# Optimization experiments

Measured on AMD Instinct MI355X. Metric: run time of the kernel, lower is better.

Reference implementation:

```python
import jax, jax.numpy as jnp
import numpy as np

B, T = 32, 4096
ATTN_DIM, ENC_DIM, DEC_DIM = 128, 512, 1024


def setup_inputs() -> dict:
    key = jax.random.key(0)
    k1, k2, k3, k4, k5, k6 = jax.random.split(key, 6)
    return {
        "query": jax.random.normal(k1, (B, DEC_DIM), dtype=jnp.float32),
        "memory": jax.random.normal(k2, (B, T, ENC_DIM), dtype=jnp.float32),
        "attention_weights_cum": jax.random.uniform(k3, (B, T), dtype=jnp.float32),
        "Wq": jax.random.normal(k4, (DEC_DIM, ATTN_DIM), dtype=jnp.float32) * (1.0 / np.sqrt(DEC_DIM)),
        "Wm": jax.random.normal(k5, (ENC_DIM, ATTN_DIM), dtype=jnp.float32) * (1.0 / np.sqrt(ENC_DIM)),
        "v": jax.random.normal(k6, (ATTN_DIM,), dtype=jnp.float32),
    }


def reference(query, memory, attention_weights_cum, Wq, Wm, v):
    # processed_query: [B, 1, A]; processed_memory: [B, T, A]
    pq = jnp.einsum('bd,da->ba', query, Wq)[:, None, :]
    pm = jnp.einsum('bte,ea->bta', memory, Wm)
    # scores: [B, T] = sum_a tanh(pq + pm) * v
    scores = jnp.einsum('bta,a->bt', jnp.tanh(pq + pm), v)
    alignments = jax.nn.softmax(scores, axis=-1)  # [B, T]
    context = jnp.einsum('bt,bte->be', alignments, memory)  # [B, E]
    return context, alignments
```

## Files before the change

### kernel.cpp

```cpp
#include <hip/hip_runtime.h>
#include <hip/hip_bf16.h>
#include <math.h>

#define B_SZ 32
#define T_SZ 4096
#define A_SZ 128
#define E_SZ 512
#define D_SZ 1024

typedef __attribute__((ext_vector_type(8))) short short8;
typedef __attribute__((ext_vector_type(4))) float f32x4;

static __device__ __forceinline__ unsigned short f32_to_bf16_rne(float x) {
    unsigned int u = __float_as_uint(x);
    unsigned int r = (u + 0x7fffu + ((u >> 16) & 1u)) >> 16;
    return (unsigned short)r;
}
static __device__ __forceinline__ float bf16_to_f32(unsigned short h) {
    return __uint_as_float(((unsigned int)h) << 16);
}

__global__ __launch_bounds__(256) void k_prep(const float* __restrict__ q,
                                              const float* __restrict__ Wq,
                                              const float* __restrict__ Wm,
                                              float* __restrict__ pq,
                                              unsigned short* __restrict__ WmTh,
                                              unsigned short* __restrict__ WmTl,
                                              float* __restrict__ ctx_out) {
    const int tid = threadIdx.x;
    if (blockIdx.x < 32) {
        const int b = blockIdx.x;
        __shared__ float ql[D_SZ];
        #pragma unroll
        for (int s = 0; s < D_SZ / 256; ++s)
            ql[s * 256 + tid] = q[b * D_SZ + s * 256 + tid];
        __syncthreads();
        if (tid < A_SZ) {
            const int a = tid;
            float acc = 0.f;
            #pragma unroll 8
            for (int d = 0; d < D_SZ; ++d)
                acc = fmaf(ql[d], Wq[d * A_SZ + a], acc);
            pq[b * A_SZ + a] = acc;
            *(float4*)(ctx_out + (size_t)b * E_SZ + tid * 4) =
                make_float4(0.f, 0.f, 0.f, 0.f);
        }
    } else {
        const int a = blockIdx.x - 32;
        for (int e = tid; e < E_SZ; e += 256) {
            float x = Wm[(size_t)e * A_SZ + a];
            unsigned short h = f32_to_bf16_rne(x);
            float r = x - bf16_to_f32(h);
            unsigned short l = f32_to_bf16_rne(r);
            WmTh[(size_t)a * E_SZ + e] = h;
            WmTl[(size_t)a * E_SZ + e] = l;
        }
    }
}

#define LDST 72

__global__ __launch_bounds__(256, 2) void k_scores_mfma(
    const float* __restrict__ mem,
    const unsigned short* __restrict__ WmTh,
    const unsigned short* __restrict__ WmTl,
    const float* __restrict__ pq,
    const float* __restrict__ v,
    float* __restrict__ scores) {
    __shared__ unsigned short Ah[128 * LDST];
    __shared__ unsigned short Al[128 * LDST];

    const int b = blockIdx.y;
    const int t0 = blockIdx.x * 128;
    const int tid = threadIdx.x;
    const int w = tid >> 6;
    const int lane = tid & 63;
    const int l16 = lane & 15;
    const int lk = lane >> 4;

    const float* memB = mem + ((size_t)b * T_SZ + t0) * E_SZ;

    float pqr[8], vr[8];
    #pragma unroll
    for (int n = 0; n < 8; ++n) {
        pqr[n] = pq[b * A_SZ + n * 16 + l16];
        vr[n]  = v[n * 16 + l16];
    }

    f32x4 acc[2][8];
    #pragma unroll
    for (int m = 0; m < 2; ++m)
        #pragma unroll
        for (int n = 0; n < 8; ++n)
            acc[m][n] = (f32x4){0.f, 0.f, 0.f, 0.f};

    for (int c = 0; c < 8; ++c) {
        const int e0 = c * 64;
        __syncthreads();
        #pragma unroll
        for (int s = 0; s < 8; ++s) {
            int idx = s * 256 + tid;
            int row = idx >> 4;
            int e4  = (idx & 15) << 2;
            float4 val = *(const float4*)(memB + (size_t)row * E_SZ + e0 + e4);
            float xs[4] = {val.x, val.y, val.z, val.w};
            unsigned int hp[2], lp[2];
            unsigned short h0 = f32_to_bf16_rne(xs[0]);
            unsigned short h1 = f32_to_bf16_rne(xs[1]);
            unsigned short h2 = f32_to_bf16_rne(xs[2]);
            unsigned short h3 = f32_to_bf16_rne(xs[3]);
            hp[0] = (unsigned int)h0 | ((unsigned int)h1 << 16);
            hp[1] = (unsigned int)h2 | ((unsigned int)h3 << 16);
            unsigned short l0 = f32_to_bf16_rne(xs[0] - bf16_to_f32(h0));
            unsigned short l1 = f32_to_bf16_rne(xs[1] - bf16_to_f32(h1));
            unsigned short l2 = f32_to_bf16_rne(xs[2] - bf16_to_f32(h2));
            unsigned short l3 = f32_to_bf16_rne(xs[3] - bf16_to_f32(h3));
            lp[0] = (unsigned int)l0 | ((unsigned int)l1 << 16);
            lp[1] = (unsigned int)l2 | ((unsigned int)l3 << 16);
            *(uint2*)&Ah[row * LDST + e4] = make_uint2(hp[0], hp[1]);
            *(uint2*)&Al[row * LDST + e4] = make_uint2(lp[0], lp[1]);
        }
        __syncthreads();

        #pragma unroll
        for (int kk = 0; kk < 2; ++kk) {
            short8 ah[2], al[2];
            #pragma unroll
            for (int m = 0; m < 2; ++m) {
                int row = w * 32 + m * 16 + l16;
                int off = row * LDST + kk * 32 + lk * 8;
                ah[m] = *(const short8*)&Ah[off];
                al[m] = *(const short8*)&Al[off];
            }
            const int eb = e0 + kk * 32 + lk * 8;
            #pragma unroll
            for (int n = 0; n < 8; ++n) {
                const int a = n * 16 + l16;
                short8 bh = *(const short8*)&WmTh[(size_t)a * E_SZ + eb];
                short8 bl = *(const short8*)&WmTl[(size_t)a * E_SZ + eb];
                acc[0][n] = __builtin_amdgcn_mfma_f32_16x16x32_bf16(ah[0], bh, acc[0][n], 0, 0, 0);
                acc[1][n] = __builtin_amdgcn_mfma_f32_16x16x32_bf16(ah[1], bh, acc[1][n], 0, 0, 0);
                acc[0][n] = __builtin_amdgcn_mfma_f32_16x16x32_bf16(al[0], bh, acc[0][n], 0, 0, 0);
                acc[1][n] = __builtin_amdgcn_mfma_f32_16x16x32_bf16(al[1], bh, acc[1][n], 0, 0, 0);
                acc[0][n] = __builtin_amdgcn_mfma_f32_16x16x32_bf16(ah[0], bl, acc[0][n], 0, 0, 0);
                acc[1][n] = __builtin_amdgcn_mfma_f32_16x16x32_bf16(ah[1], bl, acc[1][n], 0, 0, 0);
            }
        }
    }

    #pragma unroll
    for (int m = 0; m < 2; ++m) {
        float part[4] = {0.f, 0.f, 0.f, 0.f};
        #pragma unroll
        for (int n = 0; n < 8; ++n)
            #pragma unroll
            for (int r = 0; r < 4; ++r)
                part[r] += tanhf(pqr[n] + acc[m][n][r]) * vr[n];
        #pragma unroll
        for (int r = 0; r < 4; ++r) {
            #pragma unroll
            for (int off = 1; off < 16; off <<= 1)
                part[r] += __shfl_xor(part[r], off);
        }
        if (l16 == 0) {
            const int t = t0 + w * 32 + m * 16 + lk * 4;
            #pragma unroll
            for (int r = 0; r < 4; ++r)
                scores[(size_t)b * T_SZ + t + r] = part[r];
        }
    }
}

__global__ __launch_bounds__(256) void k_softmax(float* __restrict__ sc) {
    const int b = blockIdx.x;
    const int tid = threadIdx.x;
    float* row = sc + (size_t)b * T_SZ;

    float4 v4[4];
    float mx = -1e30f;
    #pragma unroll
    for (int s = 0; s < 4; ++s) {
        v4[s] = *(float4*)&row[(s * 256 + tid) * 4];
        mx = fmaxf(mx, fmaxf(fmaxf(v4[s].x, v4[s].y), fmaxf(v4[s].z, v4[s].w)));
    }
    #pragma unroll
    for (int off = 1; off < 64; off <<= 1)
        mx = fmaxf(mx, __shfl_xor(mx, off));
    __shared__ float redm[4], reds[4];
    const int wid = tid >> 6, lane = tid & 63;
    if (lane == 0) redm[wid] = mx;
    __syncthreads();
    mx = fmaxf(fmaxf(redm[0], redm[1]), fmaxf(redm[2], redm[3]));

    float sum = 0.f;
    #pragma unroll
    for (int s = 0; s < 4; ++s) {
        v4[s].x = __expf(v4[s].x - mx);
        v4[s].y = __expf(v4[s].y - mx);
        v4[s].z = __expf(v4[s].z - mx);
        v4[s].w = __expf(v4[s].w - mx);
        sum += v4[s].x + v4[s].y + v4[s].z + v4[s].w;
    }
    #pragma unroll
    for (int off = 1; off < 64; off <<= 1)
        sum += __shfl_xor(sum, off);
    if (lane == 0) reds[wid] = sum;
    __syncthreads();
    const float inv = 1.f / (reds[0] + reds[1] + reds[2] + reds[3]);
    #pragma unroll
    for (int s = 0; s < 4; ++s) {
        v4[s].x *= inv; v4[s].y *= inv; v4[s].z *= inv; v4[s].w *= inv;
        *(float4*)&row[(s * 256 + tid) * 4] = v4[s];
    }
}

__global__ __launch_bounds__(256) void k_ctx(const float* __restrict__ mem,
                                             const float* __restrict__ align,
                                             float* __restrict__ ctx) {
    const int b  = blockIdx.y;
    const int t0 = blockIdx.x * 128;
    const int tid = threadIdx.x;
    __shared__ float al[128];
    if (tid < 128) al[tid] = align[(size_t)b * T_SZ + t0 + tid];
    __syncthreads();

    const float* memB = mem + ((size_t)b * T_SZ + t0) * E_SZ;
    const int e4 = (tid & 127) * 4;
    const int th = tid >> 7;
    float4 acc = make_float4(0.f, 0.f, 0.f, 0.f);
    #pragma unroll 4
    for (int t = th; t < 128; t += 2) {
        float4 m = *(const float4*)(memB + (size_t)t * E_SZ + e4);
        const float wgt = al[t];
        acc.x = fmaf(wgt, m.x, acc.x);
        acc.y = fmaf(wgt, m.y, acc.y);
        acc.z = fmaf(wgt, m.z, acc.z);
        acc.w = fmaf(wgt, m.w, acc.w);
    }
    float* c = ctx + (size_t)b * E_SZ + e4;
    atomicAdd(c + 0, acc.x);
    atomicAdd(c + 1, acc.y);
    atomicAdd(c + 2, acc.z);
    atomicAdd(c + 3, acc.w);
}

extern "C" void kernel_launch(void* const* d_in, const int* in_sizes, int n_in,
                              void* d_out, int out_size, void* d_ws, size_t ws_size,
                              hipStream_t stream) {
    const float* query  = (const float*)d_in[0];
    const float* memory = (const float*)d_in[1];
    const float* Wq     = (const float*)d_in[3];
    const float* Wm     = (const float*)d_in[4];
    const float* v      = (const float*)d_in[5];

    float* ctx_out   = (float*)d_out;
    float* align_out = (float*)d_out + B_SZ * E_SZ;

    char* ws = (char*)d_ws;
    float* pq            = (float*)ws;
    unsigned short* WmTh = (unsigned short*)(ws + 16 * 1024);
    unsigned short* WmTl = (unsigned short*)(ws + 160 * 1024);

    k_prep<<<160, 256, 0, stream>>>(query, Wq, Wm, pq, WmTh, WmTl, ctx_out);
    k_scores_mfma<<<dim3(T_SZ / 128, B_SZ), 256, 0, stream>>>(memory, WmTh, WmTl, pq, v, align_out);
    k_softmax<<<B_SZ, 256, 0, stream>>>(align_out);
    k_ctx<<<dim3(T_SZ / 128, B_SZ), 256, 0, stream>>>(memory, align_out, ctx_out);
}
```

Baseline: 555.1 us.

## Fuse scores, chunk softmax and context into one pass with split-softmax combine

Merges the score GEMM, a per-chunk online softmax and the context accumulation into one kernel, so each 128-row memory tile is read while still hot in cache instead of being streamed again by a separate context kernel. A small combine kernel rescales the per-chunk partial contexts and normalizes the alignments, which replaces the atomics and the standalone softmax. It also stages the Wm hi/lo operands in LDS with a smaller K chunk and a higher occupancy target, and swaps tanhf for an exp-based tanh. The cost is extra workspace traffic for the partial contexts and a slightly less accurate tanh.

Result: faster. 501.8 us (-9.6%).

```diff
diff --git a/kernel.cpp b/kernel.cpp
--- a/kernel.cpp
+++ b/kernel.cpp
@@ -7,6 +7,7 @@
 #define A_SZ 128
 #define E_SZ 512
 #define D_SZ 1024
+#define NCH  32
 
 typedef __attribute__((ext_vector_type(8))) short short8;
 typedef __attribute__((ext_vector_type(4))) float f32x4;
@@ -18,6 +19,12 @@
 }
 static __device__ __forceinline__ float bf16_to_f32(unsigned short h) {
     return __uint_as_float(((unsigned int)h) << 16);
+}
+static __device__ __forceinline__ float tanh_fast(float x) {
+    float ax = fabsf(x);
+    float e  = __expf(2.f * ax);
+    float r  = 1.f - 2.f / (e + 1.f);
+    return __builtin_copysignf(r, x);
 }
 
 __global__ __launch_bounds__(256) void k_prep(const float* __restrict__ q,
@@ -25,8 +32,7 @@
                                               const float* __restrict__ Wm,
                                               float* __restrict__ pq,
                                               unsigned short* __restrict__ WmTh,
-                                              unsigned short* __restrict__ WmTl,
-                                              float* __restrict__ ctx_out) {
+                                              unsigned short* __restrict__ WmTl) {
     const int tid = threadIdx.x;
     if (blockIdx.x < 32) {
         const int b = blockIdx.x;
@@ -42,8 +48,6 @@
             for (int d = 0; d < D_SZ; ++d)
                 acc = fmaf(ql[d], Wq[d * A_SZ + a], acc);
             pq[b * A_SZ + a] = acc;
-            *(float4*)(ctx_out + (size_t)b * E_SZ + tid * 4) =
-                make_float4(0.f, 0.f, 0.f, 0.f);
         }
     } else {
         const int a = blockIdx.x - 32;
@@ -58,20 +62,30 @@
     }
 }
 
-#define LDST 72
-
-__global__ __launch_bounds__(256, 2) void k_scores_mfma(
+#define AST 36
+#define BST 40
+
+__global__ __launch_bounds__(256, 4) void k_fused(
     const float* __restrict__ mem,
     const unsigned short* __restrict__ WmTh,
     const unsigned short* __restrict__ WmTl,
     const float* __restrict__ pq,
     const float* __restrict__ v,
-    float* __restrict__ scores) {
-    __shared__ unsigned short Ah[128 * LDST];
-    __shared__ unsigned short Al[128 * LDST];
-
-    const int b = blockIdx.y;
-    const int t0 = blockIdx.x * 128;
+    float* __restrict__ scores_raw,
+    float* __restrict__ ctx_part,
+    float* __restrict__ mZ)
+{
+    __shared__ unsigned short Ah[128 * AST];
+    __shared__ unsigned short Al[128 * AST];
+    __shared__ unsigned short Bh[128 * BST];
+    __shared__ unsigned short Bl[128 * BST];
+    __shared__ float sc[128];
+    __shared__ float wbuf[128];
+    __shared__ float red[8];
+
+    const int cb = blockIdx.x;
+    const int b  = blockIdx.y;
+    const int t0 = cb * 128;
     const int tid = threadIdx.x;
     const int w = tid >> 6;
     const int lane = tid & 63;
@@ -94,57 +108,59 @@
         for (int n = 0; n < 8; ++n)
             acc[m][n] = (f32x4){0.f, 0.f, 0.f, 0.f};
 
-    for (int c = 0; c < 8; ++c) {
-        const int e0 = c * 64;
+    for (int c = 0; c < 16; ++c) {
+        const int e0 = c * 32;
         __syncthreads();
         #pragma unroll
-        for (int s = 0; s < 8; ++s) {
+        for (int s = 0; s < 4; ++s) {
             int idx = s * 256 + tid;
-            int row = idx >> 4;
-            int e4  = (idx & 15) << 2;
+            int row = idx >> 3;
+            int e4  = (idx & 7) << 2;
             float4 val = *(const float4*)(memB + (size_t)row * E_SZ + e0 + e4);
             float xs[4] = {val.x, val.y, val.z, val.w};
-            unsigned int hp[2], lp[2];
-            unsigned short h0 = f32_to_bf16_rne(xs[0]);
-            unsigned short h1 = f32_to_bf16_rne(xs[1]);
-            unsigned short h2 = f32_to_bf16_rne(xs[2]);
-            unsigned short h3 = f32_to_bf16_rne(xs[3]);
-            hp[0] = (unsigned int)h0 | ((unsigned int)h1 << 16);
-            hp[1] = (unsigned int)h2 | ((unsigned int)h3 << 16);
-            unsigned short l0 = f32_to_bf16_rne(xs[0] - bf16_to_f32(h0));
-            unsigned short l1 = f32_to_bf16_rne(xs[1] - bf16_to_f32(h1));
-            unsigned short l2 = f32_to_bf16_rne(xs[2] - bf16_to_f32(h2));
-            unsigned short l3 = f32_to_bf16_rne(xs[3] - bf16_to_f32(h3));
-            lp[0] = (unsigned int)l0 | ((unsigned int)l1 << 16);
-            lp[1] = (unsigned int)l2 | ((unsigned int)l3 << 16);
-            *(uint2*)&Ah[row * LDST + e4] = make_uint2(hp[0], hp[1]);
-            *(uint2*)&Al[row * LDST + e4] = make_uint2(lp[0], lp[1]);
+            unsigned short h[4], l[4];
+            #pragma unroll
+            for (int k = 0; k < 4; ++k) {
+                h[k] = f32_to_bf16_rne(xs[k]);
+                l[k] = f32_to_bf16_rne(xs[k] - bf16_to_f32(h[k]));
+            }
+            unsigned int hp0 = (unsigned int)h[0] | ((unsigned int)h[1] << 16);
+            unsigned int hp1 = (unsigned int)h[2] | ((unsigned int)h[3] << 16);
+            unsigned int lp0 = (unsigned int)l[0] | ((unsigned int)l[1] << 16);
+            unsigned int lp1 = (unsigned int)l[2] | ((unsigned int)l[3] << 16);
+            *(uint2*)&Ah[row * AST + e4] = make_uint2(hp0, hp1);
+            *(uint2*)&Al[row * AST + e4] = make_uint2(lp0, lp1);
+        }
+        #pragma unroll
+        for (int s = 0; s < 2; ++s) {
+            int idx = s * 256 + tid;
+            int a   = idx >> 2;
+            int es  = (idx & 3) << 3;
+            *(short8*)&Bh[a * BST + es] =
+                *(const short8*)&WmTh[(size_t)a * E_SZ + e0 + es];
+            *(short8*)&Bl[a * BST + es] =
+                *(const short8*)&WmTl[(size_t)a * E_SZ + e0 + es];
         }
         __syncthreads();
 
-        #pragma unroll
-        for (int kk = 0; kk < 2; ++kk) {
-            short8 ah[2], al[2];
-            #pragma unroll
-            for (int m = 0; m < 2; ++m) {
-                int row = w * 32 + m * 16 + l16;
-                int off = row * LDST + kk * 32 + lk * 8;
-                ah[m] = *(const short8*)&Ah[off];
-                al[m] = *(const short8*)&Al[off];
-            }
-            const int eb = e0 + kk * 32 + lk * 8;
-            #pragma unroll
-            for (int n = 0; n < 8; ++n) {
-                const int a = n * 16 + l16;
-                short8 bh = *(const short8*)&WmTh[(size_t)a * E_SZ + eb];
-                short8 bl = *(const short8*)&WmTl[(size_t)a * E_SZ + eb];
-                acc[0][n] = __builtin_amdgcn_mfma_f32_16x16x32_bf16(ah[0], bh, acc[0][n], 0, 0, 0);
-                acc[1][n] = __builtin_amdgcn_mfma_f32_16x16x32_bf16(ah[1], bh, acc[1][n], 0, 0, 0);
-                acc[0][n] = __builtin_amdgcn_mfma_f32_16x16x32_bf16(al[0], bh, acc[0][n], 0, 0, 0);
-                acc[1][n] = __builtin_amdgcn_mfma_f32_16x16x32_bf16(al[1], bh, acc[1][n], 0, 0, 0);
-                acc[0][n] = __builtin_amdgcn_mfma_f32_16x16x32_bf16(ah[0], bl, acc[0][n], 0, 0, 0);
-                acc[1][n] = __builtin_amdgcn_mfma_f32_16x16x32_bf16(ah[1], bl, acc[1][n], 0, 0, 0);
-            }
+        short8 ah[2], al[2];
+        #pragma unroll
+        for (int m = 0; m < 2; ++m) {
+            int off = (w * 32 + m * 16 + l16) * AST + lk * 8;
+            ah[m] = *(const short8*)&Ah[off];
+            al[m] = *(const short8*)&Al[off];
+        }
+        #pragma unroll
+        for (int n = 0; n < 8; ++n) {
+            int boff = (n * 16 + l16) * BST + lk * 8;
+            short8 bh = *(const short8*)&Bh[boff];
+            short8 bl = *(const short8*)&Bl[boff];
+            acc[0][n] = __builtin_amdgcn_mfma_f32_16x16x32_bf16(ah[0], bh, acc[0][n], 0, 0, 0);
+            acc[1][n] = __builtin_amdgcn_mfma_f32_16x16x32_bf16(ah[1], bh, acc[1][n], 0, 0, 0);
+            acc[0][n] = __builtin_amdgcn_mfma_f32_16x16x32_bf16(al[0], bh, acc[0][n], 0, 0, 0);
+            acc[1][n] = __builtin_amdgcn_mfma_f32_16x16x32_bf16(al[1], bh, acc[1][n], 0, 0, 0);
+            acc[0][n] = __builtin_amdgcn_mfma_f32_16x16x32_bf16(ah[0], bl, acc[0][n], 0, 0, 0);
+            acc[1][n] = __builtin_amdgcn_mfma_f32_16x16x32_bf16(ah[1], bl, acc[1][n], 0, 0, 0);
         }
     }
 
@@ -155,7 +171,7 @@
         for (int n = 0; n < 8; ++n)
             #pragma unroll
             for (int r = 0; r < 4; ++r)
-                part[r] += tanhf(pqr[n] + acc[m][n][r]) * vr[n];
+                part[r] += tanh_fast(pqr[n] + acc[m][n][r]) * vr[n];
         #pragma unroll
         for (int r = 0; r < 4; ++r) {
             #pragma unroll
@@ -163,85 +179,97 @@
                 part[r] += __shfl_xor(part[r], off);
         }
         if (l16 == 0) {
-            const int t = t0 + w * 32 + m * 16 + lk * 4;
+            const int tl = w * 32 + m * 16 + lk * 4;
             #pragma unroll
             for (int r = 0; r < 4; ++r)
-                scores[(size_t)b * T_SZ + t + r] = part[r];
-        }
-    }
-}
-
-__global__ __launch_bounds__(256) void k_softmax(float* __restrict__ sc) {
+                sc[tl + r] = part[r];
+        }
+    }
+    __syncthreads();
+
+    float mv = sc[tid & 127];
+    #pragma unroll
+    for (int off = 1; off < 64; off <<= 1)
+        mv = fmaxf(mv, __shfl_xor(mv, off));
+    if (lane == 0) red[w] = mv;
+    __syncthreads();
+    const float Mc = fmaxf(fmaxf(red[0], red[1]), fmaxf(red[2], red[3]));
+
+    float wv = 0.f;
+    if (tid < 128) {
+        wv = __expf(sc[tid] - Mc);
+        wbuf[tid] = wv;
+        scores_raw[(size_t)b * T_SZ + t0 + tid] = sc[tid];
+    }
+    float sv = wv;
+    #pragma unroll
+    for (int off = 1; off < 64; off <<= 1)
+        sv += __shfl_xor(sv, off);
+    if (lane == 0) red[4 + w] = sv;
+    __syncthreads();
+    if (tid == 0) {
+        const float Zc = red[4] + red[5];
+        mZ[(b * NCH + cb) * 2 + 0] = Mc;
+        mZ[(b * NCH + cb) * 2 + 1] = Zc;
+    }
+
+    const int e2 = tid * 2;
+    float2 a2 = make_float2(0.f, 0.f);
+    #pragma unroll 8
+    for (int t = 0; t < 128; ++t) {
+        float2 mm = *(const float2*)(memB + (size_t)t * E_SZ + e2);
+        const float wt = wbuf[t];
+        a2.x = fmaf(wt, mm.x, a2.x);
+        a2.y = fmaf(wt, mm.y, a2.y);
+    }
+    *(float2*)(ctx_part + ((size_t)cb * B_SZ + b) * E_SZ + e2) = a2;
+}
+
+__global__ __launch_bounds__(256) void k_combine(
+    const float* __restrict__ ctx_part,
+    const float* __restrict__ mZ,
+    float* __restrict__ ctx,
+    float* __restrict__ align)
+{
     const int b = blockIdx.x;
     const int tid = threadIdx.x;
-    float* row = sc + (size_t)b * T_SZ;
-
-    float4 v4[4];
-    float mx = -1e30f;
+    float mc[NCH], zc[NCH], ec[NCH];
+    float M = -1e30f;
+    #pragma unroll
+    for (int c = 0; c < NCH; ++c) {
+        float2 p = *(const float2*)(mZ + (b * NCH + c) * 2);
+        mc[c] = p.x; zc[c] = p.y;
+        M = fmaxf(M, p.x);
+    }
+    float Z = 0.f;
+    #pragma unroll
+    for (int c = 0; c < NCH; ++c) {
+        ec[c] = __expf(mc[c] - M);
+        Z = fmaf(zc[c], ec[c], Z);
+    }
+    const float invZ = 1.f / Z;
+
+    const int e2 = tid * 2;
+    float2 a2 = make_float2(0.f, 0.f);
+    #pragma unroll
+    for (int c = 0; c < NCH; ++c) {
+        float2 p = *(const float2*)(ctx_part + ((size_t)c * B_SZ + b) * E_SZ + e2);
+        a2.x = fmaf(p.x, ec[c], a2.x);
+        a2.y = fmaf(p.y, ec[c], a2.y);
+    }
+    float2 outv = make_float2(a2.x * invZ, a2.y * invZ);
+    *(float2*)(ctx + (size_t)b * E_SZ + e2) = outv;
+
+    float* row = align + (size_t)b * T_SZ;
     #pragma unroll
     for (int s = 0; s < 4; ++s) {
-        v4[s] = *(float4*)&row[(s * 256 + tid) * 4];
-        mx = fmaxf(mx, fmaxf(fmaxf(v4[s].x, v4[s].y), fmaxf(v4[s].z, v4[s].w)));
-    }
-    #pragma unroll
-    for (int off = 1; off < 64; off <<= 1)
-        mx = fmaxf(mx, __shfl_xor(mx, off));
-    __shared__ float redm[4], reds[4];
-    const int wid = tid >> 6, lane = tid & 63;
-    if (lane == 0) redm[wid] = mx;
-    __syncthreads();
-    mx = fmaxf(fmaxf(redm[0], redm[1]), fmaxf(redm[2], redm[3]));
-
-    float sum = 0.f;
-    #pragma unroll
-    for (int s = 0; s < 4; ++s) {
-        v4[s].x = __expf(v4[s].x - mx);
-        v4[s].y = __expf(v4[s].y - mx);
-        v4[s].z = __expf(v4[s].z - mx);
-        v4[s].w = __expf(v4[s].w - mx);
-        sum += v4[s].x + v4[s].y + v4[s].z + v4[s].w;
-    }
-    #pragma unroll
-    for (int off = 1; off < 64; off <<= 1)
-        sum += __shfl_xor(sum, off);
-    if (lane == 0) reds[wid] = sum;
-    __syncthreads();
-    const float inv = 1.f / (reds[0] + reds[1] + reds[2] + reds[3]);
-    #pragma unroll
-    for (int s = 0; s < 4; ++s) {
-        v4[s].x *= inv; v4[s].y *= inv; v4[s].z *= inv; v4[s].w *= inv;
-        *(float4*)&row[(s * 256 + tid) * 4] = v4[s];
-    }
-}
-
-__global__ __launch_bounds__(256) void k_ctx(const float* __restrict__ mem,
-                                             const float* __restrict__ align,
-                                             float* __restrict__ ctx) {
-    const int b  = blockIdx.y;
-    const int t0 = blockIdx.x * 128;
-    const int tid = threadIdx.x;
-    __shared__ float al[128];
-    if (tid < 128) al[tid] = align[(size_t)b * T_SZ + t0 + tid];
-    __syncthreads();
-
-    const float* memB = mem + ((size_t)b * T_SZ + t0) * E_SZ;
-    const int e4 = (tid & 127) * 4;
-    const int th = tid >> 7;
-    float4 acc = make_float4(0.f, 0.f, 0.f, 0.f);
-    #pragma unroll 4
-    for (int t = th; t < 128; t += 2) {
-        float4 m = *(const float4*)(memB + (size_t)t * E_SZ + e4);
-        const float wgt = al[t];
-        acc.x = fmaf(wgt, m.x, acc.x);
-        acc.y = fmaf(wgt, m.y, acc.y);
-        acc.z = fmaf(wgt, m.z, acc.z);
-        acc.w = fmaf(wgt, m.w, acc.w);
-    }
-    float* c = ctx + (size_t)b * E_SZ + e4;
-    atomicAdd(c + 0, acc.x);
-    atomicAdd(c + 1, acc.y);
-    atomicAdd(c + 2, acc.z);
-    atomicAdd(c + 3, acc.w);
+        float4 vv = *(float4*)&row[(s * 256 + tid) * 4];
+        vv.x = __expf(vv.x - M) * invZ;
+        vv.y = __expf(vv.y - M) * invZ;
+        vv.z = __expf(vv.z - M) * invZ;
+        vv.w = __expf(vv.w - M) * invZ;
+        *(float4*)&row[(s * 256 + tid) * 4] = vv;
+    }
 }
 
 extern "C" void kernel_launch(void* const* d_in, const int* in_sizes, int n_in,
@@ -257,12 +285,14 @@
     float* align_out = (float*)d_out + B_SZ * E_SZ;
 
     char* ws = (char*)d_ws;
-    float* pq            = (float*)ws;
-    unsigned short* WmTh = (unsigned short*)(ws + 16 * 1024);
-    unsigned short* WmTl = (unsigned short*)(ws + 160 * 1024);
-
-    k_prep<<<160, 256, 0, stream>>>(query, Wq, Wm, pq, WmTh, WmTl, ctx_out);
-    k_scores_mfma<<<dim3(T_SZ / 128, B_SZ), 256, 0, stream>>>(memory, WmTh, WmTl, pq, v, align_out);
-    k_softmax<<<B_SZ, 256, 0, stream>>>(align_out);
-    k_ctx<<<dim3(T_SZ / 128, B_SZ), 256, 0, stream>>>(memory, align_out, ctx_out);
-}
+    float*          pq       = (float*)(ws + 0);
+    unsigned short* WmTh     = (unsigned short*)(ws + 16384);
+    unsigned short* WmTl     = (unsigned short*)(ws + 147456);
+    float*          mZ       = (float*)(ws + 278528);
+    float*          ctx_part = (float*)(ws + 286720);
+
+    k_prep<<<160, 256, 0, stream>>>(query, Wq, Wm, pq, WmTh, WmTl);
+    k_fused<<<dim3(NCH, B_SZ), 256, 0, stream>>>(memory, WmTh, WmTl, pq, v,
+                                                 align_out, ctx_part, mZ);
+    k_combine<<<B_SZ, 256, 0, stream>>>(ctx_part, mZ, ctx_out, align_out);
+}
```
